# Performance work log

Hardware: AMD Instinct MI355X
Metric: run time of the kernel (lower is better)

The kernel has to match this reference:

```python
import jax, jax.numpy as jnp
import numpy as np

N_OBJS = 100          # max detections / scatter buffer size
TOP_K = 100           # top_k_n peaks per channel
KP_THRES = 0.3        # score threshold before NMS
NMS_IOU = 0.5
RESIZE_H, RESIZE_W = 1536.0, 1536.0   # resize_shape (== heatmap HxW here)
H, W = 1536, 1536


def _peak_hms(hms):
    # 3x3 stride-1 SAME max pool; keep only local maxima (Base.apply_max_pool)
    hmax = jax.lax.reduce_window(hms, -jnp.inf, jax.lax.max, (1, 3, 3, 1), (1, 1, 1, 1), 'SAME')
    return jnp.where(hms == hmax, hms, 0.0)


def _top_k_loc(hms, k):
    # per-channel top-k peak coordinates -> [b, c, k, 2] (y, x) int32
    b, h, w, c = hms.shape
    flat = jnp.transpose(hms, (0, 3, 1, 2)).reshape(b, c, h * w)
    _, idx = jax.lax.top_k(flat, k)
    return jnp.stack([idx // w, idx % w], axis=-1).astype(jnp.int32)


def _iou_matrix(boxes):
    # boxes [N,4] = (y1,x1,y2,x2)
    y1, x1, y2, x2 = boxes[:, 0], boxes[:, 1], boxes[:, 2], boxes[:, 3]
    area = jnp.maximum(y2 - y1, 0.0) * jnp.maximum(x2 - x1, 0.0)
    iy1 = jnp.maximum(y1[:, None], y1[None, :]); ix1 = jnp.maximum(x1[:, None], x1[None, :])
    iy2 = jnp.minimum(y2[:, None], y2[None, :]); ix2 = jnp.minimum(x2[:, None], x2[None, :])
    inter = jnp.maximum(iy2 - iy1, 0.0) * jnp.maximum(ix2 - ix1, 0.0)
    union = area[:, None] + area[None, :] - inter
    return inter / jnp.maximum(union, 1e-8)


def _nms_single(boxes, scores):
    # greedy single-class NMS, fixed-size (combined_non_max_suppression equivalent,
    # clip_boxes=False, score_threshold=-inf); padded slots are zeros like TF.
    order = jnp.argsort(-scores)
    boxes, scores = boxes[order], scores[order]
    n = boxes.shape[0]
    iou = _iou_matrix(boxes)
    idxs = jnp.arange(n)

    def step(suppressed, inp):
        i, iou_row = inp
        keep_i = ~suppressed[i]
        return suppressed | (keep_i & (iou_row > NMS_IOU) & (idxs > i)), keep_i

    _, keep = jax.lax.scan(step, jnp.zeros(n, bool), (idxs, iou))
    perm = jnp.argsort(jnp.where(keep, 0, 1))  # stable: compact kept to front, score order preserved
    keep_s = keep[perm]
    out_boxes = jnp.where(keep_s[:, None], boxes[perm], 0.0)
    out_scores = jnp.where(keep_s, scores[perm], 0.0)
    return out_boxes, out_scores, jnp.zeros(n, jnp.float32)


def _forward(obj_heat_map, offset_map, size_maps, origin_shapes):
    resize_shape = jnp.array([RESIZE_H, RESIZE_W], jnp.float32)
    ratio = origin_shapes / resize_shape                      # [b,2]
    hms = _peak_hms(obj_heat_map)                             # [b,H,W,2]
    b = hms.shape[0]
    coors = _top_k_loc(hms, TOP_K)                            # [b,2,K,2]
    b_coors, b_lnmks = coors[:, :1], coors[:, 1:]             # obj / nose coords
    bidx = jnp.arange(b)[:, None, None]

    # nose landmark: scores at nose-channel peaks, masked mean of coords (int mean like TF)
    nose_scores = hms[bidx, b_lnmks[..., 0], b_lnmks[..., 1], 1]     # [b,1,K]
    nose_mask = nose_scores > 0.5
    cnt = jnp.maximum(jnp.sum(nose_mask), 1)
    lnmk_mean = jnp.sum(jnp.where(nose_mask[..., None], b_lnmks, 0), axis=(0, 1, 2)) // cnt
    b_lnmks_m = lnmk_mean.reshape(b, 1, 2)                    # requires b == 1 (as in original)
    b_nose_scores = jnp.where(nose_mask, nose_scores, -1.0).reshape(b, -1)

    # boxes from sizes at object peaks
    size_vals = size_maps[bidx, b_coors[..., 0], b_coors[..., 1]]    # [b,1,K,2]
    obj_scores = hms[bidx, b_coors[..., 0], b_coors[..., 1], 0]      # [b,1,K]
    centers = b_coors.astype(jnp.float32)
    tls = jnp.maximum(centers - size_vals / 2.0, 0.0)
    brs = jnp.minimum(centers + size_vals / 2.0, resize_shape - 1.0)
    bboxes = jnp.concatenate([tls, brs], axis=-1) * jnp.tile(ratio, (1, 2))[:, None, None, :]
    bboxes, scores = bboxes[:, 0], obj_scores[:, 0]           # [b,K,4], [b,K]

    # scatter masked candidates into -1-initialized buffer (tensor_scatter_nd_update equivalent)
    mask = scores > KP_THRES
    cand = jnp.where(mask[..., None], jnp.concatenate([bboxes, scores[..., None]], -1), -1.0)
    cand = jnp.pad(cand, ((0, 0), (0, N_OBJS - TOP_K), (0, 0)), constant_values=-1.0)  # [b,N_OBJS,5]

    nb, ns, nc = jax.vmap(_nms_single)(cand[..., :4], cand[..., 4])
    box_results = jnp.where(nb == -1.0, jnp.inf, nb)
    box_results = jnp.where(box_results == 0.0, jnp.inf, box_results)  # (x - 1 == -1)
    b_bboxes = jnp.concatenate([box_results, ns[..., None], nc[..., None]], axis=-1)  # [b,N_OBJS,6]

    # offset vectors at the mean nose landmark (gather 8ch -> [b,n,4,2])
    bidx2 = jnp.arange(b)[:, None]
    off = offset_map[bidx2, b_lnmks_m[..., 0], b_lnmks_m[..., 1]].reshape(b, 1, 4, 2)
    lf = b_lnmks_m.astype(jnp.float32)
    b_ENM = (lf[:, :, None, :] - off) * ratio[:, None, None, :]
    b_lnmks_out = lf * ratio[:, None, :]
    return b_bboxes, b_lnmks_out, b_ENM, b_nose_scores


def setup_inputs() -> dict:
    key = jax.random.key(0)
    k1, k2, k3 = jax.random.split(key, 3)
    obj_heat_map = jax.random.uniform(k1, (1, H, W, 2), jnp.float32)
    offset_map = jax.random.normal(k2, (1, H, W, 8), jnp.float32) * 8.0
    size_maps = jax.random.uniform(k3, (1, H, W, 2), jnp.float32) * 128.0
    origin_shapes = jnp.array([[1080.0, 1920.0]], jnp.float32)
    return {"obj_heat_map": obj_heat_map, "offset_map": offset_map,
            "size_maps": size_maps, "origin_shapes": origin_shapes}


def reference(obj_heat_map, offset_map, size_maps, origin_shapes):
    return _forward(obj_heat_map, offset_map, size_maps, origin_shapes)
```

## Files before the change

### kernel.cpp

```cpp
#include <hip/hip_runtime.h>
#include <cstdint>

#define IW 1536
#define IH 1536
#define TOPK 100
#define CAPB 128
#define CAPT 8192
#define BF_INF16 0x7F7Fu

#define NBLK 192
#define VBTOT 576
#define LTCAP 1024

typedef unsigned u32; typedef unsigned long long u64; typedef unsigned short u16;

#define OH1   0
#define OCNT  4096
#define OSEL  4102
#define OLSD  4106
#define OBAR  4170
#define OZEND 4176
#define OSCR  4176
#define OLB   (OSCR + 2*CAPT + 2)
#define OLT   (OLB + 4*CAPB)
#define OLSDV (OLT + 4*CAPT)

__device__ __forceinline__ u32 enc16(u32 b){ b &= 0xFFFFu; return (b & 0x8000u) ? ((~b)&0xFFFFu) : (b|0x8000u); }
__device__ __forceinline__ u32 dec16(u32 e){ return (e & 0x8000u) ? (e^0x8000u) : ((~e)&0xFFFFu); }
__device__ __forceinline__ float up16(u32 b){ return __uint_as_float((b&0xFFFFu)<<16); }
__device__ __forceinline__ u16 f2bf(float f){ u32 u=__float_as_uint(f); return (u16)((u + 0x7FFFu + ((u>>16)&1u))>>16); }

__device__ __forceinline__ u32 pkmaxu16(u32 a, u32 b){
  u32 d; asm("v_pk_max_u16 %0, %1, %2" : "=v"(d) : "v"(a), "v"(b)); return d;
}

__device__ __forceinline__ void wave_sel2048(const u32* bins, u32 need, int* Dout, u32* Aout){
  int lane = threadIdx.x & 63;
  u32 s = 0;
  #pragma unroll
  for(int k=0;k<32;++k) s += bins[lane*32+k];
  u32 c = s;
  #pragma unroll
  for(int off=1;off<64;off<<=1){
    u32 v = __shfl_down(c, off, 64);
    if(lane + off < 64) c += v;
  }
  u32 cnext = __shfl_down(c, 1, 64); if(lane==63) cnext = 0u;
  u64 m = __ballot(c >= need);
  if(m == 0ull){ if(lane==0){ *Dout = 0; *Aout = 0u; } return; }
  int L = 63 - __builtin_clzll((unsigned long long)m);
  if(lane == L){
    u32 above = cnext; int D = 32*L;
    for(int b=32*L+31; b>=32*L; --b){
      u32 h = bins[b];
      if(above + h >= need){ D = b; break; }
      above += h;
    }
    *Dout = D; *Aout = above;
  }
}

union SMem {
  struct {
    u32 lh[4096];
    u32 lsdl[64];
    u64 bbuf[2][CAPB];
    u64 tbuf[2][LTCAP];
  } ab;
  struct {
    u32 h2s[2048];
    u64 keysS[CAPB];
    u32 selS[CAPB];
    u32 wbitsS[64];
    u32 lsdS[32];
    u32 hdr[10];
    float val[TOPK]; int vidx[TOPK];
    float cbox[TOPK][4]; float cscore[TOPK]; float area[TOPK];
    int sup[TOPK]; int slotv[TOPK];
    u64 nbits[2*TOPK];
  } c;
};

__device__ __forceinline__ void grid_arrive(u32* ctr){
  __hip_atomic_fetch_add(ctr, 1u, __ATOMIC_RELEASE, __HIP_MEMORY_SCOPE_AGENT);
}
__device__ __forceinline__ void grid_wait(u32* ctr, u32 target){
  while(__hip_atomic_load(ctr, __ATOMIC_RELAXED, __HIP_MEMORY_SCOPE_AGENT) < target)
    __builtin_amdgcn_s_sleep(2);
  __builtin_amdgcn_fence(__ATOMIC_ACQUIRE, "agent");
}

__global__ __launch_bounds__(1024, 4) void fused_kernel(
    const u32* __restrict__ hm, u32* __restrict__ ws,
    const u32* __restrict__ szm, const u16* __restrict__ offm,
    const u16* __restrict__ orig, u16* __restrict__ out){
  __shared__ SMem S;
  __shared__ int Dsh[2]; __shared__ u32 Ash[2];
  __shared__ u32 bcntS[2], tcntS[2], bbaseS[2], tbaseS[2];
  __shared__ int selcS, selc2S, BvS, LshS, tcS;
  __shared__ u64 suppS[2];
  __shared__ int cS, srS, scS;

  int tid = threadIdx.x, lane = tid & 63;

  for(int i=tid;i<4096;i+=1024) S.ab.lh[i]=0u;
  __syncthreads();
  for(int vb = blockIdx.x; vb < VBTOT; vb += NBLK){
    int p = (vb*1024 + tid)*4;
    int y = p / IW, x = p - y*IW;
    const u32* R1 = hm + y*IW;
    const u32* R0 = y ? R1 - IW : R1;
    const u32* R2 = (y < IH-1) ? R1 + IW : R1;
    uint4 c0 = *(const uint4*)(R0+x), c1 = *(const uint4*)(R1+x), c2 = *(const uint4*)(R2+x);
    int xl = x ? x-1 : 0, xr = (x+4 < IW) ? x+4 : IW-1;
    u32 a0[6] = {R0[xl], c0.x, c0.y, c0.z, c0.w, R0[xr]};
    u32 a1[6] = {R1[xl], c1.x, c1.y, c1.z, c1.w, R1[xr]};
    u32 a2[6] = {R2[xl], c2.x, c2.y, c2.z, c2.w, R2[xr]};
    u32 v[6], w[6];
    #pragma unroll
    for(int k=0;k<6;++k){ w[k] = pkmaxu16(a0[k], a2[k]); v[k] = pkmaxu16(w[k], a1[k]); }
    #pragma unroll
    for(int j=0;j<4;++j){
      u32 m = pkmaxu16(pkmaxu16(v[j], w[j+1]), v[j+2]);
      u32 cc = a1[j+1];
      u32 cl = cc & 0xFFFFu, chv = cc >> 16;
      if(cl  >= (m & 0xFFFFu)) atomicAdd(&S.ab.lh[enc16(cl)>>5], 1u);
      if(chv >= (m >> 16))     atomicAdd(&S.ab.lh[2048 + (enc16(chv)>>5)], 1u);
    }
  }
  __syncthreads();
  for(int i=tid;i<4096;i+=1024) if(S.ab.lh[i]) atomicAdd(&ws[OH1+i], S.ab.lh[i]);

  __syncthreads();
  if(tid==0){ grid_arrive(&ws[OBAR]); grid_wait(&ws[OBAR], (u32)NBLK); }
  __syncthreads();

  for(int i=tid;i<4096;i+=1024) S.ab.lh[i] = ws[OH1+i];
  if(tid < 64) S.ab.lsdl[tid] = 0u;
  if(tid < 2){ bcntS[tid] = 0u; tcntS[tid] = 0u; }
  __syncthreads();
  if(tid < 64)       wave_sel2048(S.ab.lh,        (u32)TOPK, &Dsh[0], &Ash[0]);
  else if(tid < 128) wave_sel2048(S.ab.lh + 2048, (u32)TOPK, &Dsh[1], &Ash[1]);
  __syncthreads();
  if(blockIdx.x == 0 && tid < 2){ ws[OSEL+tid] = (u32)Dsh[tid]; ws[OSEL+2+tid] = Ash[tid]; }

  {
    u32 thrD0 = (u32)Dsh[0] << 5, thrD1 = (u32)Dsh[1] << 5;
    u64* listBw = (u64*)(ws + OLB);
    u64* tieW   = (u64*)(ws + OLT);
    for(int vb = blockIdx.x; vb < VBTOT; vb += NBLK){
      int p = (vb*1024 + tid)*4;
      int y = p / IW, x = p - y*IW;
      const u32* R1 = hm + y*IW;
      uint4 c1v = *(const uint4*)(R1+x);
      u32 cen[4] = {c1v.x, c1v.y, c1v.z, c1v.w};
      const u32* R0 = y ? R1 - IW : R1;
      const u32* R2 = (y < IH-1) ? R1 + IW : R1;
      #pragma unroll
      for(int j=0;j<4;++j){
        u32 cc = cen[j];
        u32 cl = cc & 0xFFFFu, chv = cc >> 16;
        u32 e0 = enc16(cl), e1 = enc16(chv);
        bool cand0 = (e0 >= thrD0), cand1 = (e1 >= thrD1);
        if(!(cand0 || cand1)) continue;
        int xx = x + j;
        int xm = xx ? xx-1 : 0, xp = (xx+1 < IW) ? xx+1 : IW-1;
        u32 n0a=R0[xm], n0b=R0[xx], n0c=R0[xp];
        u32 n1a=R1[xm],             n1c=R1[xp];
        u32 n2a=R2[xm], n2b=R2[xx], n2c=R2[xp];
        u32 m0=0u, m1=0u, t;
        t=n0a&0xFFFFu; m0=t>m0?t:m0;  t=n0a>>16; m1=t>m1?t:m1;
        t=n0b&0xFFFFu; m0=t>m0?t:m0;  t=n0b>>16; m1=t>m1?t:m1;
        t=n0c&0xFFFFu; m0=t>m0?t:m0;  t=n0c>>16; m1=t>m1?t:m1;
        t=n1a&0xFFFFu; m0=t>m0?t:m0;  t=n1a>>16; m1=t>m1?t:m1;
        t=n1c&0xFFFFu; m0=t>m0?t:m0;  t=n1c>>16; m1=t>m1?t:m1;
        t=n2a&0xFFFFu; m0=t>m0?t:m0;  t=n2a>>16; m1=t>m1?t:m1;
        t=n2b&0xFFFFu; m0=t>m0?t:m0;  t=n2b>>16; m1=t>m1?t:m1;
        t=n2c&0xFFFFu; m0=t>m0?t:m0;  t=n2c>>16; m1=t>m1?t:m1;
        u32 idx = (u32)(p + j);
        u64 key0 = ((u64)e0<<32) | (u32)(~idx);
        u64 key1 = ((u64)e1<<32) | (u32)(~idx);
        if(cand0 && cl >= m0){
          if((e0>>5) > (u32)Dsh[0]){
            u32 pos = atomicAdd(&bcntS[0], 1u);
            if(pos < CAPB) S.ab.bbuf[0][pos] = key0;
          } else {
            u32 pos = atomicAdd(&tcntS[0], 1u);
            if(pos < LTCAP) S.ab.tbuf[0][pos] = key0;
            else { u32 g = atomicAdd(&ws[OCNT+4], 1u); if(g < CAPT) tieW[g] = key0; }
            atomicAdd(&S.ab.lsdl[e0 & 31u], 1u);
          }
        }
        if(cand1 && chv >= m1){
          if((e1>>5) > (u32)Dsh[1]){
            u32 pos = atomicAdd(&bcntS[1], 1u);
            if(pos < CAPB) S.ab.bbuf[1][pos] = key1;
          } else {
            u32 pos = atomicAdd(&tcntS[1], 1u);
            if(pos < LTCAP) S.ab.tbuf[1][pos] = key1;
            else { u32 g = atomicAdd(&ws[OCNT+5], 1u); if(g < CAPT) tieW[CAPT + g] = key1; }
            atomicAdd(&S.ab.lsdl[32 + (e1 & 31u)], 1u);
          }
        }
      }
    }
    __syncthreads();
    if(tid < 64) ws[OLSDV + (u32)blockIdx.x*64u + (u32)tid] = S.ab.lsdl[tid];
    if(tid >= 64 && tid < 66){
      int c2 = tid - 64;
      u32 n = bcntS[c2]; if(n > CAPB) n = CAPB;
      bcntS[c2] = n;
      bbaseS[c2] = n ? atomicAdd(&ws[OCNT+2+c2], n) : 0u;
    } else if(tid >= 66 && tid < 68){
      int ch2 = tid - 66;
      u32 n = tcntS[ch2]; if(n > LTCAP) n = LTCAP;
      tcntS[ch2] = n;
      tbaseS[ch2] = n ? atomicAdd(&ws[OCNT+4+ch2], n) : 0u;
    }
    __syncthreads();
    for(int ch2=0; ch2<2; ++ch2){
      u32 n = bcntS[ch2], base = bbaseS[ch2];
      for(u32 i=tid;i<n;i+=1024){
        u32 g = base + i;
        if(g < CAPB) listBw[ch2*CAPB + g] = S.ab.bbuf[ch2][i];
      }
      n = tcntS[ch2]; base = tbaseS[ch2];
      for(u32 i=tid;i<n;i+=1024){
        u32 g = base + i;
        if(g < CAPT) tieW[ch2*CAPT + g] = S.ab.tbuf[ch2][i];
      }
    }
  }

  __syncthreads();
  if(tid==0) grid_arrive(&ws[OBAR+1]);
  if(blockIdx.x >= 2) return;
  if(tid==0) grid_wait(&ws[OBAR+1], (u32)NBLK);
  __syncthreads();

  {
    int ch = (int)blockIdx.x;

    if(tid < 10) S.c.hdr[tid] = ws[OCNT + tid];
    if(tid < 32) S.c.lsdS[tid] = 0u;
    for(int i=tid;i<2048;i+=1024) S.c.h2s[i] = 0u;
    if(tid < 64) S.c.wbitsS[tid] = 0u;
    if(tid == 0){ selcS = 0; selc2S = 0; BvS = 0; LshS = 0; tcS = 0; }
    if(tid < TOPK){ S.c.val[tid]=0.0f; S.c.vidx[tid]=0; }
    __syncthreads();

    int nB = (int)S.c.hdr[2+ch]; if(nB > CAPB) nB = CAPB;
    int nT = (int)S.c.hdr[4+ch]; if(nT > CAPT) nT = CAPT;
    int D  = (int)S.c.hdr[6+ch];
    u32 above = S.c.hdr[8+ch];
    const u64* listB = ((const u64*)(ws + OLB)) + ch*CAPB;
    const u64* tie   = ((const u64*)(ws + OLT)) + ch*CAPT;
    u32* tidxG = ws + OSCR + ch*CAPT;

    if(tid < 512){
      int c2 = tid & 31, g = tid >> 5;
      u32 s = 0;
      for(int b = g; b < NBLK; b += 16) s += ws[OLSDV + (u32)b*64u + (u32)(ch*32 + c2)];
      if(s) atomicAdd(&S.c.lsdS[c2], s);
    }
    for(int i=tid;i<nB;i+=1024) S.c.keysS[i] = listB[i];
    __syncthreads();

    if(tid < 64){
      u32 h = (lane < 32) ? S.c.lsdS[lane] : 0u;
      u32 c = h;
      #pragma unroll
      for(int off=1;off<32;off<<=1){
        u32 v = __shfl_down(c, off, 64);
        if(lane + off < 32) c += v;
      }
      u32 need2 = (u32)TOPK - above;
      u64 m = __ballot(lane >= 1 && lane < 32 && c >= need2);
      if(lane == 0){
        LshS = m ? (63 - __builtin_clzll((unsigned long long)m)) : 0;
        selcS = nB;
      }
    }
    __syncthreads();
    u32 thr = ((u32)D<<5) | (u32)LshS;
    float tval = up16(dec16(thr));

    for(int base2=0; base2<nT; base2+=1024){
      int i = base2 + tid;
      bool act = (i < nT);
      u64 k = 0; u32 e = 0, idx = 0;
      if(act){ k = tie[i]; e = (u32)(k>>32); idx = ~(u32)(k & 0xFFFFFFFFu); }
      if(act && e > thr){
        int pos = atomicAdd(&selcS, 1); if(pos < CAPB) S.c.keysS[pos] = k;
      }
      bool isT = act && (e == thr);
      u64 mk = __ballot(isT);
      if(mk){
        u32 cw = __popcll(mk), b;
        if(lane==0) b = (u32)atomicAdd(&tcS, (int)cw);
        b = __shfl(b, 0);
        if(isT){
          u32 pos = b + __popcll(mk & ((1ull<<lane)-1ull));
          if(pos < CAPT) tidxG[pos] = idx;
        }
      }
      if(isT) atomicAdd(&S.c.h2s[idx>>11], 1u);
    }
    __syncthreads();

    int nA = selcS; if(nA > CAPB) nA = CAPB; if(nA > TOPK) nA = TOPK;
    int need = TOPK - nA;
    if(tid < nA){
      u64 kreg = S.c.keysS[tid];
      int r = 0;
      for(int j=0;j<nA;++j) r += (S.c.keysS[j] > kreg);
      if(r < TOPK){
        S.c.val[r] = up16(dec16((u32)(kreg>>32)));
        S.c.vidx[r] = (int)(~(u32)(kreg & 0xFFFFFFFFu));
      }
    }
    if(tid < 64){
      const u32* hh = S.c.h2s;
      int base = lane*32;
      u32 s = 0;
      #pragma unroll
      for(int k2=0;k2<32;++k2) s += hh[base+k2];
      u32 c = s;
      #pragma unroll
      for(int off=1;off<64;off<<=1){
        u32 v = __shfl_up(c, off, 64);
        if(lane >= off) c += v;
      }
      u64 m = __ballot(need > 0 && c >= (u32)need);
      int L = m ? (int)(__ffsll((unsigned long long)m) - 1) : -1;
      if(L >= 0 && lane == L){
        u32 hb[32];
        #pragma unroll
        for(int k2=0;k2<32;++k2) hb[k2] = hh[base+k2];
        u32 cum2 = c - s;
        int Bsel = base;
        #pragma unroll
        for(int k2=0;k2<32;++k2){
          if(cum2 + hb[k2] >= (u32)need){ Bsel = base+k2; break; }
          cum2 += hb[k2];
        }
        BvS = Bsel;
      }
    }
    __syncthreads();

    int B = BvS;
    int tc = tcS; if(tc > CAPT) tc = CAPT;
    if(need > 0){
      for(int i=tid;i<tc;i+=1024){
        u32 idx = tidxG[i];
        int b = (int)(idx>>11);
        if(b < B){
          int pos = atomicAdd(&selc2S, 1);
          if(pos < CAPB) S.c.selS[pos] = idx;
        } else if(b == B){
          atomicOr(&S.c.wbitsS[(idx&2047)>>5], 1u<<(idx&31));
        }
      }
    }
    __syncthreads();

    int sc = selc2S; if(sc > CAPB) sc = CAPB;
    if(need > 0 && tid < sc){
      u32 v = S.c.selS[tid];
      int r = 0;
      for(int j=0;j<sc;++j) r += (S.c.selS[j] < v);
      if(nA + r < TOPK){ S.c.val[nA+r] = tval; S.c.vidx[nA+r] = (int)v; }
    }
    if(need > 0 && tid < 64){
      u32 bits = S.c.wbitsS[tid];
      u32 cnt = __popc(bits);
      u32 incl = cnt;
      #pragma unroll
      for(int off=1;off<64;off<<=1){
        u32 v = __shfl_up(incl, off, 64);
        if(lane >= off) incl += v;
      }
      int excl = (int)(incl - cnt);
      int rem = need - sc;
      int pos = nA + sc + excl;
      int j = 0;
      while(bits){
        int l = __ffs(bits) - 1; bits &= bits - 1;
        if(excl + j < rem && pos + j < TOPK){
          S.c.val[pos+j] = tval;
          S.c.vidx[pos+j] = (int)(((u32)B<<11) | ((u32)tid<<5) | (u32)l);
        }
        ++j;
      }
    }
    __syncthreads();

    float ry = up16(orig[0]) / 1536.0f;
    float rx = up16(orig[1]) / 1536.0f;

    if(ch == 1){
      if(tid == 0){ cS = 0; srS = 0; scS = 0; }
      __syncthreads();
      if(tid < TOPK && S.c.val[tid] > 0.5f){
        atomicAdd(&cS, 1);
        atomicAdd(&srS, S.c.vidx[tid] / IW);
        atomicAdd(&scS, S.c.vidx[tid] % IW);
      }
      if(tid < TOPK) out[610 + tid] = f2bf(S.c.val[tid] > 0.5f ? S.c.val[tid] : -1.0f);
      __syncthreads();
      if(tid == 0){
        int c = cS < 1 ? 1 : cS;
        int meanr = srS / c, meanc = scS / c;
        float lfy = (float)meanr, lfx = (float)meanc;
        out[600] = f2bf(lfy * ry);
        out[601] = f2bf(lfx * rx);
        const u16* op = offm + ((size_t)meanr*IW + meanc)*8;
        for(int p=0;p<4;++p){
          out[602 + p*2 + 0] = f2bf((lfy - up16(op[p*2+0])) * ry);
          out[602 + p*2 + 1] = f2bf((lfx - up16(op[p*2+1])) * rx);
        }
      }
      return;
    }

    if(tid < TOPK){
      int idx = S.c.vidx[tid];
      int r = idx / IW, c = idx - r*IW;
      float score = S.c.val[tid];
      u32 sz = szm[idx];
      float sy = up16(sz), sx = up16(sz>>16);
      float cy = (float)r, cx = (float)c;
      float tly = fmaxf(cy - sy*0.5f, 0.0f);
      float tlx = fmaxf(cx - sx*0.5f, 0.0f);
      float bry = fminf(cy + sy*0.5f, 1535.0f);
      float brx = fminf(cx + sx*0.5f, 1535.0f);
      bool mk = score > 0.3f;
      float b0 = mk ? tly*ry : -1.0f;
      float b1 = mk ? tlx*rx : -1.0f;
      float b2 = mk ? bry*ry : -1.0f;
      float b3 = mk ? brx*rx : -1.0f;
      S.c.cbox[tid][0]=b0; S.c.cbox[tid][1]=b1; S.c.cbox[tid][2]=b2; S.c.cbox[tid][3]=b3;
      S.c.cscore[tid] = mk ? score : -1.0f;
      S.c.area[tid] = fmaxf(b2-b0,0.0f) * fmaxf(b3-b1,0.0f);
    }
    if(tid < 2*TOPK) S.c.nbits[tid] = 0ull;
    __syncthreads();

    for(int t=tid; t<TOPK*TOPK; t+=512){
      int i = t / TOPK, j = t - i*TOPK;
      if(j > i){
        float iy1 = fmaxf(S.c.cbox[i][0], S.c.cbox[j][0]);
        float ix1 = fmaxf(S.c.cbox[i][1], S.c.cbox[j][1]);
        float iy2 = fminf(S.c.cbox[i][2], S.c.cbox[j][2]);
        float ix2 = fminf(S.c.cbox[i][3], S.c.cbox[j][3]);
        float inter = fmaxf(iy2-iy1,0.0f) * fmaxf(ix2-ix1,0.0f);
        float uni = (S.c.area[i] + S.c.area[j]) - inter;
        if(inter / fmaxf(uni, 1e-8f) > 0.5f)
          atomicOr(&S.c.nbits[i*2 + (j>>6)], 1ull << (j&63));
      }
    }
    __syncthreads();
    if(tid == 0){
      u64 s0 = 0ull, s1 = 0ull;
      for(int base=0;base<TOPK;base+=10){
        u64 buf[20];
        #pragma unroll
        for(int k=0;k<20;++k) buf[k] = S.c.nbits[2*base+k];
        #pragma unroll
        for(int k=0;k<10;++k){
          int i = base+k;
          bool su = (i<64) ? ((s0>>i)&1ull) : ((s1>>(i-64))&1ull);
          if(!su){ s0 |= buf[2*k]; s1 |= buf[2*k+1]; }
        }
      }
      suppS[0] = s0; suppS[1] = s1;
    }
    __syncthreads();
    if(tid < TOPK) S.c.sup[tid] = (int)((suppS[tid>>6] >> (tid&63)) & 1ull);
    __syncthreads();

    if(tid < TOPK){
      int kbefore = 0, sbefore = 0, ktot = 0;
      for(int j=0;j<TOPK;++j){
        int sj = S.c.sup[j];
        ktot += (1 - sj);
        if(j < tid){ kbefore += (1 - sj); sbefore += sj; }
      }
      int slot = S.c.sup[tid] ? (ktot + sbefore) : kbefore;
      S.c.slotv[slot] = tid;
    }
    __syncthreads();

    if(tid < TOPK){
      int s = S.c.slotv[tid];
      bool ks = !S.c.sup[s];
      u16 row[6];
      if(ks){
        for(int d=0;d<4;++d){
          float v = S.c.cbox[s][d];
          row[d] = (v == -1.0f || v == 0.0f) ? (u16)BF_INF16 : f2bf(v);
        }
        row[4] = f2bf(S.c.cscore[s]);
      } else {
        for(int d=0;d<4;++d) row[d] = (u16)BF_INF16;
        row[4] = 0;
      }
      row[5] = 0;
      for(int d=0;d<6;++d) out[tid*6 + d] = row[d];
    }
  }
}

extern "C" void kernel_launch(void* const* d_in, const int* in_sizes, int n_in,
                              void* d_out, int out_size, void* d_ws, size_t ws_size,
                              hipStream_t stream) {
  const u32* heat = (const u32*)d_in[0];
  const u16* offm = (const u16*)d_in[1];
  const u32* szm  = (const u32*)d_in[2];
  const u16* orig = (const u16*)d_in[3];
  u16* out = (u16*)d_out;
  u32* ws = (u32*)d_ws;

  hipMemsetAsync(ws, 0, OZEND*sizeof(u32), stream);
  fused_kernel<<<NBLK, 1024, 0, stream>>>(heat, ws, szm, offm, orig, out);
}
```

Before: 171.4 us.

## Replicate global histogram, keep tie indices in LDS, widen NMS IoU stride

The global 4096-bin histogram merge now spreads blocks across four replicas with a per-block rotated bin order, which is meant to cut atomic contention on the same addresses. After the grid barrier, each block sums the four replicas when it reads the histogram back. The per-channel tie-index scratch moves from global memory into LDS, which raises the LDS footprint of the select stage. The IoU pair loop stride goes from 512 to 1024, so threads above 512 no longer repeat the same pairs.

```diff
diff --git a/kernel.cpp b/kernel.cpp
--- a/kernel.cpp
+++ b/kernel.cpp
@@ -11,17 +11,16 @@
 #define NBLK 192
 #define VBTOT 576
 #define LTCAP 1024
+#define NREP 4
 
 typedef unsigned u32; typedef unsigned long long u64; typedef unsigned short u16;
 
 #define OH1   0
-#define OCNT  4096
-#define OSEL  4102
-#define OLSD  4106
-#define OBAR  4170
-#define OZEND 4176
-#define OSCR  4176
-#define OLB   (OSCR + 2*CAPT + 2)
+#define OCNT  (NREP*4096)
+#define OSEL  (OCNT+6)
+#define OBAR  (OCNT+10)
+#define OZEND (OCNT+16)
+#define OLB   OZEND
 #define OLT   (OLB + 4*CAPB)
 #define OLSDV (OLT + 4*CAPT)
 
@@ -68,6 +67,7 @@
     u64 tbuf[2][LTCAP];
   } ab;
   struct {
+    u32 tidxS[CAPT];
     u32 h2s[2048];
     u64 keysS[CAPB];
     u32 selS[CAPB];
@@ -129,13 +129,21 @@
     }
   }
   __syncthreads();
-  for(int i=tid;i<4096;i+=1024) if(S.ab.lh[i]) atomicAdd(&ws[OH1+i], S.ab.lh[i]);
+  {
+    u32 rot = ((u32)blockIdx.x * 97u) & 4095u;
+    u32* H = ws + OH1 + ((u32)blockIdx.x & (NREP-1))*4096u;
+    for(int i=tid;i<4096;i+=1024){
+      u32 b = ((u32)i + rot) & 4095u;
+      if(S.ab.lh[b]) atomicAdd(&H[b], S.ab.lh[b]);
+    }
+  }
 
   __syncthreads();
   if(tid==0){ grid_arrive(&ws[OBAR]); grid_wait(&ws[OBAR], (u32)NBLK); }
   __syncthreads();
 
-  for(int i=tid;i<4096;i+=1024) S.ab.lh[i] = ws[OH1+i];
+  for(int i=tid;i<4096;i+=1024)
+    S.ab.lh[i] = ws[OH1+i] + ws[OH1+4096+i] + ws[OH1+8192+i] + ws[OH1+12288+i];
   if(tid < 64) S.ab.lsdl[tid] = 0u;
   if(tid < 2){ bcntS[tid] = 0u; tcntS[tid] = 0u; }
   __syncthreads();
@@ -255,7 +263,6 @@
     u32 above = S.c.hdr[8+ch];
     const u64* listB = ((const u64*)(ws + OLB)) + ch*CAPB;
     const u64* tie   = ((const u64*)(ws + OLT)) + ch*CAPT;
-    u32* tidxG = ws + OSCR + ch*CAPT;
 
     if(tid < 512){
       int c2 = tid & 31, g = tid >> 5;
@@ -301,7 +308,7 @@
         b = __shfl(b, 0);
         if(isT){
           u32 pos = b + __popcll(mk & ((1ull<<lane)-1ull));
-          if(pos < CAPT) tidxG[pos] = idx;
+          if(pos < CAPT) S.c.tidxS[pos] = idx;
         }
       }
       if(isT) atomicAdd(&S.c.h2s[idx>>11], 1u);
@@ -353,7 +360,7 @@
     int tc = tcS; if(tc > CAPT) tc = CAPT;
     if(need > 0){
       for(int i=tid;i<tc;i+=1024){
-        u32 idx = tidxG[i];
+        u32 idx = S.c.tidxS[i];
         int b = (int)(idx>>11);
         if(b < B){
           int pos = atomicAdd(&selc2S, 1);
@@ -447,7 +454,7 @@
     if(tid < 2*TOPK) S.c.nbits[tid] = 0ull;
     __syncthreads();
 
-    for(int t=tid; t<TOPK*TOPK; t+=512){
+    for(int t=tid; t<TOPK*TOPK; t+=1024){
       int i = t / TOPK, j = t - i*TOPK;
       if(j > i){
         float iy1 = fmaxf(S.c.cbox[i][0], S.c.cbox[j][0]);
```

Measured after the change: 167.4 us (median of 2 runs). 1.02x faster.
